# Kernel tuning notes

Measured on AMD Instinct MI355X. Metric: run time of the kernel, lower is better.

Reference implementation:

```python
import jax, jax.numpy as jnp
import numpy as np

D = 1024          # feature dim (x_dim)
C = 32            # n classes (way)
SHOTS = 32
N_SUP = C * SHOTS
Q = 1024
REG = 0.5         # reg_param


def setup_inputs() -> dict:
    key = jax.random.key(0)
    ks = jax.random.split(key, 5)
    support_x = jax.random.normal(ks[0], (N_SUP, D), dtype=jnp.float32)
    query_x = jax.random.normal(ks[1], (Q, D), dtype=jnp.float32)
    labels_idx = (jnp.arange(N_SUP, dtype=jnp.int32) % C)  # every class present, equal shots
    m = jax.random.normal(ks[2], (1, D), dtype=jnp.float32) * 0.01
    kappa = jnp.float32(0.1)
    nu = jnp.float32(D)
    triu_diag = jnp.ones((D,), dtype=jnp.float32)
    triu_lower = jnp.eye(D, dtype=jnp.float32) + 0.01 * jax.random.normal(ks[3], (D, D), dtype=jnp.float32)
    return {"support_x": support_x, "query_x": query_x, "labels_idx": labels_idx,
            "m": m, "kappa": kappa, "nu": nu,
            "triu_diag": triu_diag, "triu_lower": triu_lower}


def _metaqda_fb(support_x, query_x, labels_idx, m, kappa, nu, triu_diag, triu_lower):
    onehot = jax.nn.one_hot(labels_idx, C, dtype=support_x.dtype)      # [N, C]
    Nj = jnp.sum(onehot, axis=0)                                       # [C]
    kappa_ = jnp.abs(kappa) + 1e-6
    nu_ = jnp.maximum(nu, jnp.float32(D - 1 + 1e-6))

    # Cholesky-factor prior scatter matrix: L @ L^T
    lower_mask = jnp.tril(jnp.ones((D, D), dtype=support_x.dtype), k=-1)
    L = jnp.diag(jnp.abs(triu_diag)) + triu_lower * lower_mask
    prior_S = L @ L.T                                                  # [D, D]

    # per-class sums (replaces python loop of rank-1 outer products with GEMMs)
    sum_x = onehot.T @ support_x                                       # [C, D]
    mean_x = sum_x / Nj[:, None]
    # sum_n x x^T per class: contract through [N,C,D] intermediate
    SXX = jnp.einsum('nc,nd,ne->cde', onehot, support_x, support_x)    # [C, D, D]

    kN = kappa_ + Nj                                                   # [C]
    mu = (kappa_ / kN)[:, None] * m + (Nj / kN)[:, None] * mean_x      # [C, D]

    mm = m.T @ m                                                       # [D, D]  (self_outer of [1,D])
    mumu = jnp.einsum('cd,ce->cde', mu, mu)                            # [C, D, D]
    S = prior_S[None] + SXX + kappa_ * mm[None] - kN[:, None, None] * mumu

    scale = (kN + 1.0) / ((nu_ + Nj - D + 1.0) * kN)                   # [C]
    sigma = S * scale[:, None, None]                                   # [C, D, D]

    sigma_inv = (1.0 - REG) * jnp.linalg.inv(sigma) + REG * jnp.eye(D, dtype=sigma.dtype)

    common = nu_ + Nj + 1.0 - D                                        # [C]
    _, logdet = jnp.linalg.slogdet(sigma)
    bias = (jax.lax.lgamma(0.5 * (common + D)) - jax.lax.lgamma(0.5 * common)
            - 0.5 * D * jnp.log(common) - 0.5 * logdet)                # [C]

    diff = query_x[:, None, :] - mu[None, :, :]                        # [Q, C, D]
    dist = jnp.einsum('qcd,cde,qce->qc', diff, sigma_inv, diff)        # [Q, C]
    preds = bias[None, :] - 0.5 * (common + D)[None, :] * jnp.log1p(dist / common[None, :])
    return preds


def reference(support_x, query_x, labels_idx, m, kappa, nu, triu_diag, triu_lower):
    return _metaqda_fb(support_x, query_x, labels_idx, m, kappa, nu, triu_diag, triu_lower)
```

## Files before the change

### kernel.cpp

```cpp
#include <hip/hip_runtime.h>
#include <math.h>

#define Dk 1024
#define Ck 32
#define Nk 1024
#define Qk 1024
#define REGP 0.5f
#define NB 64
#define NROWSV (Qk + Nk + Ck + 1)

#define CO_KAPPA 0
#define CO_NU    1
#define CO_NJ    2
#define CO_KN    34
#define CO_SCALE 66
#define CO_COMMON 98
#define CO_COEF  130
#define CO_BIASA 162
#define CO_BIASF 200

#define O_P    0u
#define O_W    2162688u
#define O_T    3211264u
#define O_MU   3473408u
#define O_QM   3506176u
#define O_MB   3538944u
#define O_MI   3578112u
#define O_QNY  3617280u
#define O_QNO  3618304u
#define O_MUN  3619328u
#define O_GMM  3619360u
#define O_EX   3619392u
#define O_CONS 3619408u
#define O_CIDX 3619664u
#define O_YH   3652432u
#define O_YM   4733776u
#define O_YL   5815120u
#define O_WH   6896464u
#define O_WM   7420752u
#define O_WL   7945040u
#define O_OH   8469328u
#define O_OM   9550672u
#define O_OL   10632016u

#define WS_DECL \
    float* P     = Wbuf + O_P;    (void)P; \
    float* W     = Wbuf + O_W;    (void)W; \
    float* Tb    = Wbuf + O_T;    (void)Tb; \
    float* QM    = Wbuf + O_QM;   (void)QM; \
    float* Mbuf  = Wbuf + O_MB;   (void)Mbuf; \
    float* Minv  = Wbuf + O_MI;   (void)Minv; \
    float* qny   = Wbuf + O_QNY;  (void)qny; \
    float* qno   = Wbuf + O_QNO;  (void)qno; \
    float* mun2o = Wbuf + O_MUN;  (void)mun2o; \
    float* gmm   = Wbuf + O_GMM;  (void)gmm; \
    float* extraf= Wbuf + O_EX;   (void)extraf; \
    float* cons  = Wbuf + O_CONS; (void)cons; \
    int*   cidx  = (int*)(Wbuf + O_CIDX); (void)cidx; \
    ushort* sYh = (ushort*)(Wbuf + O_YH); (void)sYh; \
    ushort* sYm = (ushort*)(Wbuf + O_YM); (void)sYm; \
    ushort* sYl = (ushort*)(Wbuf + O_YL); (void)sYl; \
    ushort* sWh = (ushort*)(Wbuf + O_WH); (void)sWh; \
    ushort* sWm = (ushort*)(Wbuf + O_WM); (void)sWm; \
    ushort* sWl = (ushort*)(Wbuf + O_WL); (void)sWl; \
    ushort* sOh = (ushort*)(Wbuf + O_OH); (void)sOh; \
    ushort* sOm = (ushort*)(Wbuf + O_OM); (void)sOm; \
    ushort* sOl = (ushort*)(Wbuf + O_OL); (void)sOl;

typedef __attribute__((ext_vector_type(8))) __bf16 bf16x8;
typedef __attribute__((ext_vector_type(4))) float f32x4;

#define MFMA(a, b, c) __builtin_amdgcn_mfma_f32_16x16x32_bf16(a, b, c, 0, 0, 0)

__device__ __forceinline__ ushort f2bf(float x) {
    unsigned u = __float_as_uint(x);
    return (ushort)((u + 0x7FFFu + ((u >> 16) & 1u)) >> 16);
}
__device__ __forceinline__ float bf2f(ushort h) {
    return __uint_as_float(((unsigned)h) << 16);
}
__device__ __forceinline__ void split1(float x, ushort& h, ushort& m, ushort& l) {
    h = f2bf(x);
    float r1 = x - bf2f(h);
    m = f2bf(r1);
    l = f2bf(r1 - bf2f(m));
}
__device__ __forceinline__ void split_store4(ushort* ph, ushort* pm, ushort* pl,
                                             size_t o, float4 v) {
    float vv[4] = {v.x, v.y, v.z, v.w};
    ushort4 H, M, L;
    ushort* Hp = (ushort*)&H; ushort* Mp = (ushort*)&M; ushort* Lp = (ushort*)&L;
#pragma unroll
    for (int c = 0; c < 4; ++c) split1(vv[c], Hp[c], Mp[c], Lp[c]);
    *(ushort4*)(ph + o) = H;
    *(ushort4*)(pm + o) = M;
    *(ushort4*)(pl + o) = L;
}

__device__ __forceinline__ float wave_red(float s) {
#pragma unroll
    for (int o = 32; o > 0; o >>= 1) s += __shfl_down(s, o, 64);
    return s;
}

#define LDSB3(c, r, k8) ((c) * 5120 + (r) * 40 + (k8))
#define LDS_HW3 15360

__device__ __forceinline__ void b_fetch3(bf16x8* rb,
                                         const ushort* Bh, const ushort* Bm, const ushort* Bl,
                                         int bRow0, int kcol, int t) {
#pragma unroll
    for (int u = 0; u < 6; ++u) {
        int comp = u >> 1;
        int idx = ((u & 1) << 8) + t;
        int row = idx >> 2, kg = idx & 3;
        const ushort* Bs = (comp == 0) ? Bh : ((comp == 1) ? Bm : Bl);
        rb[u] = *(const bf16x8*)(Bs + (size_t)(bRow0 + row) * 1024 + kcol + kg * 8);
    }
}
__device__ __forceinline__ void b_store3(ushort* lds, const bf16x8* rb, int t) {
#pragma unroll
    for (int u = 0; u < 6; ++u) {
        int comp = u >> 1;
        int idx = ((u & 1) << 8) + t;
        int row = idx >> 2, kg = idx & 3;
        *(bf16x8*)(lds + LDSB3(comp, row, kg * 8)) = rb[u];
    }
}
__device__ __forceinline__ void a_fetch3(bf16x8 af[4][3],
                                         const ushort* Ah, const ushort* Am, const ushort* Al,
                                         int arowT, int aRowMax, int kcol, int lk) {
    bf16x8 z = {};
#pragma unroll
    for (int rf = 0; rf < 4; ++rf) {
        int gr = arowT + rf * 16;
        bool ok = gr < aRowMax;
#pragma unroll
        for (int c = 0; c < 3; ++c) {
            const ushort* As = (c == 0) ? Ah : ((c == 1) ? Am : Al);
            af[rf][c] = ok ? *(const bf16x8*)(As + (size_t)gr * 1024 + kcol + lk * 8) : z;
        }
    }
}

__device__ __forceinline__ void tile_compute3(const ushort* lds, f32x4 acc[4][4],
                                              bf16x8 af[4][3], int bcol0, int lr, int lk) {
#pragma unroll
    for (int cf = 0; cf < 4; ++cf) {
        int brow = bcol0 + cf * 16 + lr;
        bf16x8 bh = *(const bf16x8*)(lds + LDSB3(0, brow, lk * 8));
        bf16x8 bm = *(const bf16x8*)(lds + LDSB3(1, brow, lk * 8));
        bf16x8 bl = *(const bf16x8*)(lds + LDSB3(2, brow, lk * 8));
#pragma unroll
        for (int rf = 0; rf < 4; ++rf) {
            f32x4 a = acc[rf][cf];
            a = MFMA(af[rf][0], bh, a);
            a = MFMA(af[rf][0], bm, a);
            a = MFMA(af[rf][1], bh, a);
            a = MFMA(af[rf][0], bl, a);
            a = MFMA(af[rf][2], bh, a);
            a = MFMA(af[rf][1], bm, a);
            acc[rf][cf] = a;
        }
    }
}

__device__ __forceinline__ void tile_gemm3(
    ushort* lds, f32x4 acc[4][4],
    const ushort* Ah, const ushort* Am, const ushort* Al, int aRow0, int aRowMax,
    const ushort* Bh, const ushort* Bm, const ushort* Bl, int bRow0,
    int kbase, int ksteps, int t)
{
    const int w = t >> 6, lr = t & 15, lk = (t >> 4) & 3;
    const int arowT = aRow0 + (w >> 1) * 64 + lr;
    const int bcol0 = (w & 1) * 64;
    bf16x8 rb[6], afc[4][3], afn[4][3];
    b_fetch3(rb, Bh, Bm, Bl, bRow0, kbase * 32, t);
    a_fetch3(afc, Ah, Am, Al, arowT, aRowMax, kbase * 32, lk);
    b_store3(lds, rb, t);
    __syncthreads();
    for (int kt = 0; kt < ksteps; ++kt) {
        if (kt + 1 < ksteps) {
            b_fetch3(rb, Bh, Bm, Bl, bRow0, (kbase + kt + 1) * 32, t);
            a_fetch3(afn, Ah, Am, Al, arowT, aRowMax, (kbase + kt + 1) * 32, lk);
        }
        tile_compute3(lds, acc, afc, bcol0, lr, lk);
        __syncthreads();
        if (kt + 1 < ksteps) {
            b_store3(lds, rb, t);
#pragma unroll
            for (int rf = 0; rf < 4; ++rf)
#pragma unroll
                for (int c = 0; c < 3; ++c) afc[rf][c] = afn[rf][c];
        }
        __syncthreads();
    }
}

__device__ __forceinline__ void fetch4(float4* reg, const float* src, int ld,
                                       int rowbase, int rowmax, int colbase, int t) {
#pragma unroll
    for (int u = 0; u < 4; ++u) {
        int slot = t + u * 256;
        int r = slot >> 4, c4 = slot & 15;
        int gr = rowbase + r;
        reg[u] = (gr < rowmax) ? *(const float4*)(src + (size_t)gr * ld + colbase + c4 * 4)
                               : make_float4(0.f, 0.f, 0.f, 0.f);
    }
}
__device__ __forceinline__ void stT(float* dst, const float4* reg, int t) {
#pragma unroll
    for (int u = 0; u < 4; ++u) {
        int slot = t + u * 256;
        int r = slot >> 4, c4 = slot & 15;
        dst[(c4 * 4 + 0) * 68 + r] = reg[u].x;
        dst[(c4 * 4 + 1) * 68 + r] = reg[u].y;
        dst[(c4 * 4 + 2) * 68 + r] = reg[u].z;
        dst[(c4 * 4 + 3) * 68 + r] = reg[u].w;
    }
}
__device__ __forceinline__ void stN(float* dst, const float4* reg, int t) {
#pragma unroll
    for (int u = 0; u < 4; ++u) {
        int slot = t + u * 256;
        int r = slot >> 4, c4 = slot & 15;
        *(float4*)(dst + r * 68 + c4 * 4) = reg[u];
    }
}
__device__ __forceinline__ void gemm16(const float* At, const float* Bt,
                                       float acc[4][4], int tx, int ty) {
#pragma unroll 4
    for (int kk = 0; kk < NB; ++kk) {
        float4 a = *(const float4*)(At + kk * 68 + ty * 4);
        float4 b = *(const float4*)(Bt + kk * 68 + tx * 4);
        float av[4] = {a.x, a.y, a.z, a.w};
        float bv[4] = {b.x, b.y, b.z, b.w};
#pragma unroll
        for (int r = 0; r < 4; ++r)
#pragma unroll
            for (int s = 0; s < 4; ++s) acc[r][s] += av[r] * bv[s];
    }
}
__device__ __forceinline__ void mm_task(
    const float* aSrc, int aLd, int aRow, int aRowMax, int aCol, int aRowStep, int aColStep,
    const float* bSrc, int bLd, int bRow, int bRowMax, int bCol, int bRowStep, int bColStep,
    bool bTrans, int k0, int k1,
    float acc[4][4], float* smA, float* smB, int t, int tx, int ty)
{
    float4 ra[4], rb[4];
    fetch4(ra, aSrc, aLd, aRow + k0 * aRowStep, aRowMax, aCol + k0 * aColStep, t);
    fetch4(rb, bSrc, bLd, bRow + k0 * bRowStep, bRowMax, bCol + k0 * bColStep, t);
    stT(smA, ra, t);
    if (bTrans) stT(smB, rb, t); else stN(smB, rb, t);
    __syncthreads();
    for (int kt = k0; kt < k1; ++kt) {
        if (kt + 1 < k1) {
            fetch4(ra, aSrc, aLd, aRow + (kt + 1) * aRowStep, aRowMax, aCol + (kt + 1) * aColStep, t);
            fetch4(rb, bSrc, bLd, bRow + (kt + 1) * bRowStep, bRowMax, bCol + (kt + 1) * bColStep, t);
        }
        gemm16(smA, smB, acc, tx, ty);
        __syncthreads();
        if (kt + 1 < k1) {
            stT(smA, ra, t);
            if (bTrans) stT(smB, rb, t); else stN(smB, rb, t);
        }
        __syncthreads();
    }
}

__global__ __launch_bounds__(64) void k_tri0(const float* td, const float* tl, float* Wbuf) {
    __shared__ __align__(16) float smem[4416];
    WS_DECL
    const int t = threadIdx.x;
    int b0 = blockIdx.x * NB;
    float* LT   = smem;
    float* dinv = smem + 4352;
    for (int idx = t; idx < 64 * 64; idx += 64) {
        int m = idx >> 6, i = idx & 63;
        LT[i * 68 + m] = (m > i) ? tl[(size_t)(b0 + m) * Dk + b0 + i] : 0.f;
    }
    dinv[t] = 1.f / fabsf(td[b0 + t]);
    __syncthreads();
    const int j = t;
    float r[64];
#pragma unroll
    for (int m = 0; m < 64; ++m) r[m] = (m == j) ? 1.f : 0.f;
#pragma unroll
    for (int i = 0; i < 64; ++i) {
        float x = r[i] * dinv[i];
        r[i] = x;
#pragma unroll
        for (int g = (i >> 2); g < 16; ++g) {
            float4 lt = *(const float4*)&LT[i * 68 + g * 4];
            r[g * 4 + 0] -= lt.x * x;
            r[g * 4 + 1] -= lt.y * x;
            r[g * 4 + 2] -= lt.z * x;
            r[g * 4 + 3] -= lt.w * x;
        }
    }
#pragma unroll
    for (int i = 0; i < 64; ++i)
        W[(size_t)(b0 + i) * Dk + b0 + j] = r[i];
}

__global__ __launch_bounds__(256) void k_p0(const float* qx, const int* labels,
                                            const float* mvec, const float* kappa,
                                            const float* nu, const float* td,
                                            float* Wbuf) {
    __shared__ __align__(16) float sX[512];
    WS_DECL
    float* Yo32 = Wbuf;
    const int t = threadIdx.x;
    const int lane = t & 63, wv = t >> 6;
    const int tau = blockIdx.x;

    if (tau == 0) {
        int* scnt = (int*)sX;
        if (t < Ck) scnt[t] = 0;
        __syncthreads();
        for (int n = t; n < Nk; n += 256) {
            int l = labels[n];
            int pos = atomicAdd(&scnt[l], 1);
            cidx[l * Nk + pos] = n;
        }
        __syncthreads();
        if (t < Ck) {
            float kap = fabsf(kappa[0]) + 1e-6f;
            float nu_ = fmaxf(nu[0], (float)(Dk - 1) + 1e-6f);
            float Njf = (float)scnt[t];
            float kN = kap + Njf;
            if (t == 0) { cons[CO_KAPPA] = kap; cons[CO_NU] = nu_; }
            cons[CO_NJ + t] = Njf;
            cons[CO_KN + t] = kN;
            cons[CO_SCALE + t] = (kN + 1.0f) / ((nu_ + Njf - (float)Dk + 1.0f) * kN);
            float common = nu_ + Njf + 1.0f - (float)Dk;
            cons[CO_COMMON + t] = common;
            cons[CO_COEF + t] = 0.5f * (common + (float)Dk);
            cons[CO_BIASA + t] = lgammaf(0.5f * (common + (float)Dk)) - lgammaf(0.5f * common)
                                 - 0.5f * (float)Dk * logf(common);
        }
    } else if (tau == 1) {
        float s = 0.f;
        for (int i = t; i < Dk; i += 256) s += logf(fabsf(td[i]));
        s = wave_red(s);
        if (lane == 0) sX[wv] = s;
        __syncthreads();
        if (t == 0) extraf[0] = 2.f * (sX[0] + sX[1] + sX[2] + sX[3]);
    } else if (tau < 5) {
        int base = (tau - 2) * 13056;
        for (int i = t; i < 13056 && base + i < 39168; i += 256) Mbuf[base + i] = 0.f;
    } else if (tau == 5) {
        if (t < 32) { mun2o[t] = 0.f; gmm[t] = 0.f; }
        for (int i = t; i < 8192; i += 256)
            ((float4*)QM)[i] = make_float4(0, 0, 0, 0);
        if (t < 256) ((float4*)qny)[t] = make_float4(0, 0, 0, 0);
    } else if (tau < 70) {
        int rbase = (tau - 6) * 16;
        for (int j2 = wv; j2 < 16; j2 += 4) {
            const float* row = qx + (size_t)(rbase + j2) * Dk;
            float s = 0.f;
            for (int d = lane; d < Dk; d += 64) { float v = row[d]; s += v * v; }
            s = wave_red(s);
            if (lane == 0) qno[rbase + j2] = s;
        }
    } else if (tau < 134) {
        int rbase = (tau - 70) * 16;
        for (int j2 = 0; j2 < 16; ++j2) {
            int r = rbase + j2;
            float4 v = ((const float4*)(qx + (size_t)r * Dk))[t];
            split_store4(sYh, sYm, sYl, (size_t)r * 1024 + (size_t)t * 4, v);
        }
    } else if (tau == 134) {
        float4 v = ((const float4*)mvec)[t];
        split_store4(sYh, sYm, sYl, (size_t)2080 * 1024 + (size_t)t * 4, v);
    } else {
        int rbase = (tau - 135) * 16;
        for (int j2 = 0; j2 < 16; ++j2)
            ((float4*)(Yo32 + (size_t)(rbase + j2) * 1024))[t] = make_float4(0, 0, 0, 0);
    }
}

__global__ __launch_bounds__(256) void k_p1(const float* sx, const float* mvec,
                                            const float* tl, float* Wbuf) {
    __shared__ __align__(16) float smem[8704];
    WS_DECL
    const int t = threadIdx.x;
    const int lane = t & 63, wv = t >> 6;
    const int tau = blockIdx.x;
    if (tau < 128) {
        float* sX = smem;
        int c = tau >> 2;
        int d = ((tau & 3) << 8) + t;
        int Nj = (int)cons[CO_NJ + c];
        float kap = cons[CO_KAPPA], kN = cons[CO_KN + c];
        float acc = 0.f;
        for (int s = 0; s < Nj; ++s) acc += sx[(size_t)cidx[c * Nk + s] * Dk + d];
        float muv = (kap * mvec[d] + acc) / kN;
        size_t o = (size_t)(2048 + c) * 1024 + d;
        ushort h, m_, l_;
        split1(muv, h, m_, l_);
        sYh[o] = h; sYm[o] = m_; sYl[o] = l_;
        float s2 = wave_red(muv * muv);
        if (lane == 0) sX[wv] = s2;
        __syncthreads();
        if (t == 0) atomicAdd(&mun2o[c], sX[0] + sX[1] + sX[2] + sX[3]);
    } else if (tau < 192) {
        int rbase = (tau - 128) * 16;
        for (int j = 0; j < 16; ++j) {
            int n = rbase + j;
            int srcrow = cidx[(n >> 5) * Nk + (n & 31)];
            float4 v = ((const float4*)(sx + (size_t)srcrow * Dk))[t];
            split_store4(sYh, sYm, sYl, (size_t)(1024 + n) * 1024 + (size_t)t * 4, v);
        }
    } else {
        float* smA = smem;
        float* smB = smem + 4352;
        const int tx = t & 15, ty = t >> 4;
        const int BIG = 1 << 30;
        int pb = (tau - 192) * 128;
        float acc[4][4] = {};
        mm_task(tl, Dk, pb + 64, BIG, pb, 0, NB,
                W, Dk, pb, BIG, pb, NB, 0, false, 0, 1,
                acc, smA, smB, t, tx, ty);
        {
            float4 ra[4];
            fetch4(ra, W, Dk, pb + 64, BIG, pb + 64, t);
#pragma unroll
            for (int r = 0; r < 4; ++r)
#pragma unroll
                for (int s = 0; s < 4; ++s)
                    smB[(ty * 4 + r) * 68 + tx * 4 + s] = acc[r][s];
            stT(smA, ra, t);
        }
        __syncthreads();
        float acc2[4][4] = {};
        gemm16(smA, smB, acc2, tx, ty);
        __syncthreads();
#pragma unroll
        for (int r = 0; r < 4; ++r)
#pragma unroll
            for (int s = 0; s < 4; ++s)
                W[(size_t)(pb + 64 + ty * 4 + r) * Dk + pb + tx * 4 + s] = -acc2[r][s];
    }
}

__global__ __launch_bounds__(256) void k_tr_a(const float* tl, float* Wbuf, int h, int ht) {
    __shared__ __align__(16) float smem[8704];
    float* smA = smem;
    float* smB = smem + 4352;
    WS_DECL
    const int t = threadIdx.x;
    const int tx = t & 15, ty = t >> 4;
    const int BIG = 1 << 30;
    int tau = blockIdx.x;
    int p = tau / (ht * ht), rr = tau % (ht * ht);
    int i = rr / ht, j = rr % ht;
    int pb = p * 2 * h;
    float acc[4][4] = {};
    mm_task(tl, Dk, pb + h + i * NB, BIG, pb, 0, NB,
            W, Dk, pb, BIG, pb + j * NB, NB, 0, false, 0, ht,
            acc, smA, smB, t, tx, ty);
    float* Tp = Tb + (size_t)p * h * h;
#pragma unroll
    for (int r = 0; r < 4; ++r)
#pragma unroll
        for (int s = 0; s < 4; ++s)
            Tp[(size_t)(i * NB + ty * 4 + r) * h + j * NB + tx * 4 + s] = acc[r][s];
}

__global__ __launch_bounds__(256) void k_tr_b(float* Wbuf, int h, int ht) {
    __shared__ __align__(16) float smem[8704];
    float* smA = smem;
    float* smB = smem + 4352;
    WS_DECL
    const int t = threadIdx.x;
    const int tx = t & 15, ty = t >> 4;
    const int BIG = 1 << 30;
    int tau = blockIdx.x;
    int p = tau / (ht * ht), rr = tau % (ht * ht);
    int i = rr / ht, j = rr % ht;
    int pb = p * 2 * h;
    const float* Tp = Tb + (size_t)p * h * h;
    float acc[4][4] = {};
    mm_task(W, Dk, pb + h + i * NB, BIG, pb + h, 0, NB,
            Tp, h, 0, BIG, j * NB, NB, 0, false, 0, ht,
            acc, smA, smB, t, tx, ty);
#pragma unroll
    for (int r = 0; r < 4; ++r)
#pragma unroll
        for (int s = 0; s < 4; ++s)
            W[(size_t)(pb + h + i * NB + ty * 4 + r) * Dk + pb + j * NB + tx * 4 + s] = -acc[r][s];
}

__global__ __launch_bounds__(256) void k_cvtw(float* Wbuf) {
    WS_DECL
    const int t = threadIdx.x;
#pragma unroll
    for (int u = 0; u < 4; ++u) {
        unsigned g = blockIdx.x * 1024u + u * 256u + t;
        int row = g >> 8, col4 = (g & 255) * 4;
        float4 v = ((const float4*)W)[g];
        if (col4 + 0 > row) v.x = 0.f;
        if (col4 + 1 > row) v.y = 0.f;
        if (col4 + 2 > row) v.z = 0.f;
        if (col4 + 3 > row) v.w = 0.f;
        split_store4(sWh, sWm, sWl, (size_t)g * 4, v);
    }
}

__global__ __launch_bounds__(256) void k_yg(float* Wbuf) {
    __shared__ __align__(16) ushort lds[LDS_HW3];
    WS_DECL
    float* Yo32 = Wbuf;
    const int t = threadIdx.x;
    int b = blockIdx.x;
    int xcd = b & 7, pos = b >> 3;
    int e = (xcd < 4) ? xcd * 43 + pos : 172 + (xcd - 4) * 42 + pos;
    int q = e / 17, rt = e % 17;
    int jt2, kc;
    if (q < 4)       { jt2 = 7; kc = q; }
    else if (q < 8)  { jt2 = 6; kc = q - 4; }
    else if (q < 11) { jt2 = 5; kc = q - 8; }
    else if (q < 14) { jt2 = 4; kc = q - 11; }
    else if (q < 16) { jt2 = 3; kc = q - 14; }
    else if (q < 18) { jt2 = 2; kc = q - 16; }
    else if (q == 18){ jt2 = 1; kc = 0; }
    else             { jt2 = 0; kc = 0; }
    int ksteps = min(8, 4 * (jt2 + 1) - kc * 8);
    f32x4 acc[4][4] = {};
    tile_gemm3(lds, acc, sYh, sYm, sYl, rt * 128, 2081,
               sWh, sWm, sWl, jt2 * 128, kc * 8, ksteps, t);
    const int w = t >> 6, lr = t & 15, lk = (t >> 4) & 3;
#pragma unroll
    for (int rf = 0; rf < 4; ++rf)
#pragma unroll
        for (int cf = 0; cf < 4; ++cf)
#pragma unroll
            for (int r = 0; r < 4; ++r) {
                int grow = rt * 128 + (w >> 1) * 64 + rf * 16 + lk * 4 + r;
                if (grow < NROWSV)
                    atomicAdd(&Yo32[(size_t)grow * 1024 + jt2 * 128 + (w & 1) * 64 + cf * 16 + lr],
                              acc[rf][cf][r]);
            }
}

__global__ __launch_bounds__(256) void k_cvto(float* Wbuf) {
    __shared__ float sred[16];
    WS_DECL
    float* Yo32 = Wbuf;
    const int t = threadIdx.x;
    const int lane = t & 63, wv = t >> 6;
    int rbase = blockIdx.x * 4;
    float4 vv[4];
#pragma unroll
    for (int j = 0; j < 4; ++j) {
        int r = rbase + j;
        float4 v = ((const float4*)(Yo32 + (size_t)r * 1024))[t];
        vv[j] = v;
        split_store4(sOh, sOm, sOl, (size_t)r * 1024 + (size_t)t * 4, v);
    }
    if (rbase < 1024) {
#pragma unroll
        for (int j = 0; j < 4; ++j) {
            float4 v = vv[j];
            float s = v.x * v.x + v.y * v.y + v.z * v.z + v.w * v.w;
            s = wave_red(s);
            if (lane == 0) sred[wv * 4 + j] = s;
        }
        __syncthreads();
        if (t < 4)
            qny[rbase + t] = sred[t] + sred[4 + t] + sred[8 + t] + sred[12 + t];
    }
    if (rbase < 1088) {
#pragma unroll
        for (int j = 0; j < 4; ++j)
            ((float4*)(Yo32 + (size_t)(rbase + j) * 1024))[t] = make_float4(0, 0, 0, 0);
    }
}

__global__ __launch_bounds__(256) void k_p4m(float* Wbuf) {
    __shared__ __align__(16) ushort lds[LDS_HW3];
    WS_DECL
    const int t = threadIdx.x;
    int b = blockIdx.x;
    int e = (b & 7) * 40 + (b >> 3);
    const int w = t >> 6, lr = t & 15, lk = (t >> 4) & 3;
    f32x4 acc[4][4] = {};
    if (e < 288) {
        int qt2 = e / 36, rem = e % 36;
        int mt = rem >> 2, kc = rem & 3;
        tile_gemm3(lds, acc, sOh, sOm, sOl, 1024 + mt * 128, 2081,
                   sOh, sOm, sOl, qt2 * 128, kc * 8, 8, t);
#pragma unroll
        for (int rf = 0; rf < 4; ++rf)
#pragma unroll
            for (int cf = 0; cf < 4; ++cf)
#pragma unroll
                for (int r = 0; r < 4; ++r) {
                    int n = mt * 128 + (w >> 1) * 64 + rf * 16 + lk * 4 + r;
                    if (n < Nk + Ck + 1)
                        atomicAdd(&P[(size_t)n * 1024 + qt2 * 128 + (w & 1) * 64 + cf * 16 + lr],
                                  acc[rf][cf][r]);
                }
    } else {
        int f = e - 288;
        int qt2 = f >> 2, kc = f & 3;
        tile_gemm3(lds, acc, sYh, sYm, sYl, 2048, 2080,
                   sYh, sYm, sYl, qt2 * 128, kc * 8, 8, t);
#pragma unroll
        for (int rf = 0; rf < 4; ++rf)
#pragma unroll
            for (int cf = 0; cf < 4; ++cf)
#pragma unroll
                for (int r = 0; r < 4; ++r) {
                    int rq = (w >> 1) * 64 + rf * 16 + lk * 4 + r;
                    if (rq < 32)
                        atomicAdd(&QM[(size_t)rq * 1024 + qt2 * 128 + (w & 1) * 64 + cf * 16 + lr],
                                  acc[rf][cf][r]);
                }
    }
}

__global__ __launch_bounds__(256) void k_gram(float* Wbuf) {
    __shared__ __align__(16) float smA[34 * 68];
    WS_DECL
    const int t = threadIdx.x;
    const int tau = blockIdx.x;
    int c = tau >> 2, kc = tau & 3;
    float accg[5];
    int iu[5], ju[5];
#pragma unroll
    for (int u = 0; u < 5; ++u) {
        int e = t + u * 256;
        iu[u] = e / 34; ju[u] = e - iu[u] * 34;
        accg[u] = 0.f;
    }
    for (int kt = kc * 4; kt < kc * 4 + 4; ++kt) {
        for (int e2 = t; e2 < 34 * NB; e2 += 256) {
            int i = e2 >> 6, k = e2 & 63;
            int yr = (i < 32) ? (Qk + c * 32 + i) : ((i == 32) ? (Qk + Nk + c) : (Qk + Nk + Ck));
            size_t o = (size_t)yr * 1024 + kt * NB + k;
            smA[i * 68 + k] = bf2f(sOh[o]) + bf2f(sOm[o]) + bf2f(sOl[o]);
        }
        __syncthreads();
#pragma unroll
        for (int u = 0; u < 5; ++u) {
            int e = t + u * 256;
            if (e < 1156) {
                float s = 0.f;
                for (int k = 0; k < NB; ++k) s += smA[iu[u] * 68 + k] * smA[ju[u] * 68 + k];
                accg[u] += s;
            }
        }
        __syncthreads();
    }
#pragma unroll
    for (int u = 0; u < 5; ++u) {
        int e = t + u * 256;
        if (e < 1156)
            atomicAdd(&Mbuf[c * 1224 + iu[u] * 36 + ju[u]], accg[u]);
    }
}

__global__ __launch_bounds__(64) void k_p5(float* Wbuf) {
    __shared__ __align__(16) float A[34 * 36];
    WS_DECL
    const int t = threadIdx.x;
    const int c = blockIdx.x;
    float kN = cons[CO_KN + c], kap = cons[CO_KAPPA];
    for (int e = t; e < 34 * 34; e += 64) {
        int i = e / 34, j = e - i * 34;
        A[i * 36 + j] = Mbuf[c * 1224 + i * 36 + j];
    }
    __syncthreads();
    if (t == 0) {
        gmm[c] = A[32 * 36 + 32];
        A[32 * 36 + 32] += -1.f / kN;
        A[33 * 36 + 33] += 1.f / kap;
    }
    if (t < 32) A[t * 36 + t] += 1.f;
    __syncthreads();
    float ldacc = 0.f;
    for (int j = 0; j < 34; ++j) {
        float piv = A[j * 36 + j];
        float pinv = 1.f / piv;
        if (t == 0) ldacc += logf(fabsf(piv));
        if (t < 34 && t != j) A[j * 36 + t] *= pinv;
        __syncthreads();
        if (t < 34) {
            if (t != j) {
                float f = A[t * 36 + j];
                float4* rowT = (float4*)(A + t * 36);
                const float4* rowJ = (const float4*)(A + j * 36);
#pragma unroll
                for (int k4 = 0; k4 < 8; ++k4) {
                    float4 rv = rowT[k4], pv = rowJ[k4];
                    rv.x -= f * pv.x; rv.y -= f * pv.y;
                    rv.z -= f * pv.z; rv.w -= f * pv.w;
                    rowT[k4] = rv;
                }
                A[t * 36 + 32] -= f * A[j * 36 + 32];
                A[t * 36 + 33] -= f * A[j * 36 + 33];
                A[t * 36 + j] = -f * pinv;
            } else {
                A[j * 36 + j] = pinv;
            }
        }
        __syncthreads();
    }
    for (int e = t; e < 34 * 34; e += 64) {
        int i = e / 34, j = e - i * 34;
        Minv[c * 1224 + i * 36 + j] = A[i * 36 + j];
    }
    if (t == 0) {
        float scale = cons[CO_SCALE + c];
        float logdet = (float)Dk * logf(scale) + extraf[0] + logf(kN) + logf(kap) + ldacc;
        cons[CO_BIASF + c] = cons[CO_BIASA + c] - 0.5f * logdet;
    }
}

__global__ __launch_bounds__(256) void k_p6(float* Wbuf, float* out) {
    __shared__ __align__(16) float smem[3904];
    float* Mi  = smem;
    float* wL  = smem + 1200;
    float* gsm = smem + 3520;
    float* red = smem + 3520 + 128;
    WS_DECL
    const int t = threadIdx.x;
    const int tau = blockIdx.x;
    int qt = tau >> 5, c = tau & 31;
    for (int e = t; e < 34 * 34; e += 256) {
        int i = e / 34, j = e - i * 34;
        Mi[i * 35 + j] = Minv[c * 1224 + i * 36 + j];
    }
    if (t < 34)
        gsm[t] = (t < 32) ? Mbuf[c * 1224 + t * 36 + 32]
                          : ((t == 32) ? gmm[c] : Mbuf[c * 1224 + 33 * 36 + 32]);
    __syncthreads();
    for (int e = t; e < 34 * NB; e += 256) {
        int i = e >> 6, qq = e & 63;
        int prow = (i < 32) ? (c * 32 + i) : ((i == 32) ? (Nk + c) : (Nk + Ck));
        wL[i * 68 + qq] = P[(size_t)prow * Qk + qt * NB + qq] - gsm[i];
    }
    __syncthreads();
    {
        int q = t & 63, part = t >> 6;
        int start = (part < 2) ? part * 9 : 18 + (part - 2) * 8;
        int cnt = (part < 2) ? 9 : 8;
        float partial = 0.f;
        for (int i = start; i < start + cnt; ++i) {
            float v = 0.f;
            for (int j = 0; j < 34; ++j) v += Mi[i * 35 + j] * wL[j * 68 + q];
            partial += v * wL[i * 68 + q];
        }
        red[part * 64 + q] = partial;
    }
    __syncthreads();
    if (t < 64) {
        int q = t;
        float quad = red[q] + red[64 + q] + red[128 + q] + red[192 + q];
        int qg = qt * NB + q;
        float w32 = wL[32 * 68 + q];
        float ydist2 = qny[qg] - 2.f * w32 - gmm[c];
        float dd = qno[qg] + mun2o[c] - 2.f * QM[(size_t)c * Qk + qg];
        float scale = cons[CO_SCALE + c], common = cons[CO_COMMON + c];
        float dist = (1.f - REGP) / scale * (ydist2 - quad) + REGP * dd;
        out[(size_t)qg * Ck + c] = cons[CO_BIASF + c] - cons[CO_COEF + c] * log1pf(dist / common);
    }
}

extern "C" void kernel_launch(void* const* d_in, const int* in_sizes, int n_in,
                              void* d_out, int out_size, void* d_ws, size_t ws_size,
                              hipStream_t stream) {
    const float* sx = (const float*)d_in[0];
    const float* qx = (const float*)d_in[1];
    const int* labels = (const int*)d_in[2];
    const float* mvec = (const float*)d_in[3];
    const float* kappa = (const float*)d_in[4];
    const float* nu = (const float*)d_in[5];
    const float* td = (const float*)d_in[6];
    const float* tl = (const float*)d_in[7];
    float* W = (float*)d_ws;
    float* out = (float*)d_out;

    hipLaunchKernelGGL(k_p0, dim3(267), dim3(256), 0, stream,
                       qx, labels, mvec, kappa, nu, td, W);
    hipLaunchKernelGGL(k_tri0, dim3(16), dim3(64), 0, stream, td, tl, W);
    hipLaunchKernelGGL(k_p1, dim3(200), dim3(256), 0, stream, sx, mvec, tl, W);
    for (int l = 2; l <= 4; ++l) {
        int h = 32 << l, ht = h >> 6, pairs = 16 >> l;
        int nt = pairs * ht * ht;
        hipLaunchKernelGGL(k_tr_a, dim3(nt), dim3(256), 0, stream, tl, W, h, ht);
        hipLaunchKernelGGL(k_tr_b, dim3(nt), dim3(256), 0, stream, W, h, ht);
    }
    hipLaunchKernelGGL(k_cvtw, dim3(256), dim3(256), 0, stream, W);
    hipLaunchKernelGGL(k_yg, dim3(340), dim3(256), 0, stream, W);
    hipLaunchKernelGGL(k_cvto, dim3(528), dim3(256), 0, stream, W);
    hipLaunchKernelGGL(k_p4m, dim3(320), dim3(256), 0, stream, W);
    hipLaunchKernelGGL(k_gram, dim3(128), dim3(256), 0, stream, W);
    hipLaunchKernelGGL(k_p5, dim3(32), dim3(64), 0, stream, W);
    hipLaunchKernelGGL(k_p6, dim3(512), dim3(256), 0, stream, W, out);
}
```

Measured before the change: 373.7 us.

## Move query-row norm reduction into gram kernel and drop XCD block remapping

```diff
diff --git a/kernel.cpp b/kernel.cpp
--- a/kernel.cpp
+++ b/kernel.cpp
@@ -353,7 +353,6 @@
         if (t < 32) { mun2o[t] = 0.f; gmm[t] = 0.f; }
         for (int i = t; i < 8192; i += 256)
             ((float4*)QM)[i] = make_float4(0, 0, 0, 0);
-        if (t < 256) ((float4*)qny)[t] = make_float4(0, 0, 0, 0);
     } else if (tau < 70) {
         int rbase = (tau - 6) * 16;
         for (int j2 = wv; j2 < 16; j2 += 4) {
@@ -513,9 +512,7 @@
     WS_DECL
     float* Yo32 = Wbuf;
     const int t = threadIdx.x;
-    int b = blockIdx.x;
-    int xcd = b & 7, pos = b >> 3;
-    int e = (xcd < 4) ? xcd * 43 + pos : 172 + (xcd - 4) * 42 + pos;
+    int e = blockIdx.x;
     int q = e / 17, rt = e % 17;
     int jt2, kc;
     if (q < 4)       { jt2 = 7; kc = q; }
@@ -545,31 +542,15 @@
 }
 
 __global__ __launch_bounds__(256) void k_cvto(float* Wbuf) {
-    __shared__ float sred[16];
     WS_DECL
     float* Yo32 = Wbuf;
     const int t = threadIdx.x;
-    const int lane = t & 63, wv = t >> 6;
     int rbase = blockIdx.x * 4;
-    float4 vv[4];
 #pragma unroll
     for (int j = 0; j < 4; ++j) {
         int r = rbase + j;
         float4 v = ((const float4*)(Yo32 + (size_t)r * 1024))[t];
-        vv[j] = v;
         split_store4(sOh, sOm, sOl, (size_t)r * 1024 + (size_t)t * 4, v);
-    }
-    if (rbase < 1024) {
-#pragma unroll
-        for (int j = 0; j < 4; ++j) {
-            float4 v = vv[j];
-            float s = v.x * v.x + v.y * v.y + v.z * v.z + v.w * v.w;
-            s = wave_red(s);
-            if (lane == 0) sred[wv * 4 + j] = s;
-        }
-        __syncthreads();
-        if (t < 4)
-            qny[rbase + t] = sred[t] + sred[4 + t] + sred[8 + t] + sred[12 + t];
     }
     if (rbase < 1088) {
 #pragma unroll
@@ -582,13 +563,12 @@
     __shared__ __align__(16) ushort lds[LDS_HW3];
     WS_DECL
     const int t = threadIdx.x;
-    int b = blockIdx.x;
-    int e = (b & 7) * 40 + (b >> 3);
+    int e = blockIdx.x;
     const int w = t >> 6, lr = t & 15, lk = (t >> 4) & 3;
     f32x4 acc[4][4] = {};
     if (e < 288) {
-        int qt2 = e / 36, rem = e % 36;
-        int mt = rem >> 2, kc = rem & 3;
+        int tile = e >> 2, kc = e & 3;
+        int mt = tile >> 3, qt2 = tile & 7;
         tile_gemm3(lds, acc, sOh, sOm, sOl, 1024 + mt * 128, 2081,
                    sOh, sOm, sOl, qt2 * 128, kc * 8, 8, t);
 #pragma unroll
@@ -625,40 +605,56 @@
     __shared__ __align__(16) float smA[34 * 68];
     WS_DECL
     const int t = threadIdx.x;
+    const int lane = t & 63, wv = t >> 6;
     const int tau = blockIdx.x;
-    int c = tau >> 2, kc = tau & 3;
-    float accg[5];
-    int iu[5], ju[5];
-#pragma unroll
-    for (int u = 0; u < 5; ++u) {
-        int e = t + u * 256;
-        iu[u] = e / 34; ju[u] = e - iu[u] * 34;
-        accg[u] = 0.f;
-    }
-    for (int kt = kc * 4; kt < kc * 4 + 4; ++kt) {
-        for (int e2 = t; e2 < 34 * NB; e2 += 256) {
-            int i = e2 >> 6, k = e2 & 63;
-            int yr = (i < 32) ? (Qk + c * 32 + i) : ((i == 32) ? (Qk + Nk + c) : (Qk + Nk + Ck));
-            size_t o = (size_t)yr * 1024 + kt * NB + k;
-            smA[i * 68 + k] = bf2f(sOh[o]) + bf2f(sOm[o]) + bf2f(sOl[o]);
-        }
-        __syncthreads();
+    if (tau < 128) {
+        int c = tau >> 2, kc = tau & 3;
+        float accg[5];
+        int iu[5], ju[5];
 #pragma unroll
         for (int u = 0; u < 5; ++u) {
             int e = t + u * 256;
-            if (e < 1156) {
-                float s = 0.f;
-                for (int k = 0; k < NB; ++k) s += smA[iu[u] * 68 + k] * smA[ju[u] * 68 + k];
-                accg[u] += s;
+            iu[u] = e / 34; ju[u] = e - iu[u] * 34;
+            accg[u] = 0.f;
+        }
+        for (int kt = kc * 4; kt < kc * 4 + 4; ++kt) {
+            for (int e2 = t; e2 < 34 * NB; e2 += 256) {
+                int i = e2 >> 6, k = e2 & 63;
+                int yr = (i < 32) ? (Qk + c * 32 + i) : ((i == 32) ? (Qk + Nk + c) : (Qk + Nk + Ck));
+                size_t o = (size_t)yr * 1024 + kt * NB + k;
+                smA[i * 68 + k] = bf2f(sOh[o]) + bf2f(sOm[o]) + bf2f(sOl[o]);
             }
-        }
-        __syncthreads();
-    }
-#pragma unroll
-    for (int u = 0; u < 5; ++u) {
-        int e = t + u * 256;
-        if (e < 1156)
-            atomicAdd(&Mbuf[c * 1224 + iu[u] * 36 + ju[u]], accg[u]);
+            __syncthreads();
+#pragma unroll
+            for (int u = 0; u < 5; ++u) {
+                int e = t + u * 256;
+                if (e < 1156) {
+                    float s = 0.f;
+                    for (int k = 0; k < NB; ++k) s += smA[iu[u] * 68 + k] * smA[ju[u] * 68 + k];
+                    accg[u] += s;
+                }
+            }
+            __syncthreads();
+        }
+#pragma unroll
+        for (int u = 0; u < 5; ++u) {
+            int e = t + u * 256;
+            if (e < 1156)
+                atomicAdd(&Mbuf[c * 1224 + iu[u] * 36 + ju[u]], accg[u]);
+        }
+    } else {
+        int rbase = (tau - 128) * 16;
+        for (int j = wv; j < 16; j += 4) {
+            size_t ro = (size_t)(rbase + j) * 1024;
+            float s = 0.f;
+            for (int d = lane; d < Dk; d += 64) {
+                size_t o = ro + d;
+                float v = bf2f(sOh[o]) + bf2f(sOm[o]) + bf2f(sOl[o]);
+                s += v * v;
+            }
+            s = wave_red(s);
+            if (lane == 0) qny[rbase + j] = s;
+        }
     }
 }
 
@@ -783,9 +779,9 @@
     float* W = (float*)d_ws;
     float* out = (float*)d_out;
 
+    hipLaunchKernelGGL(k_tri0, dim3(16), dim3(64), 0, stream, td, tl, W);
     hipLaunchKernelGGL(k_p0, dim3(267), dim3(256), 0, stream,
                        qx, labels, mvec, kappa, nu, td, W);
-    hipLaunchKernelGGL(k_tri0, dim3(16), dim3(64), 0, stream, td, tl, W);
     hipLaunchKernelGGL(k_p1, dim3(200), dim3(256), 0, stream, sx, mvec, tl, W);
     for (int l = 2; l <= 4; ++l) {
         int h = 32 << l, ht = h >> 6, pairs = 16 >> l;
@@ -797,7 +793,7 @@
     hipLaunchKernelGGL(k_yg, dim3(340), dim3(256), 0, stream, W);
     hipLaunchKernelGGL(k_cvto, dim3(528), dim3(256), 0, stream, W);
     hipLaunchKernelGGL(k_p4m, dim3(320), dim3(256), 0, stream, W);
-    hipLaunchKernelGGL(k_gram, dim3(128), dim3(256), 0, stream, W);
+    hipLaunchKernelGGL(k_gram, dim3(192), dim3(256), 0, stream, W);
     hipLaunchKernelGGL(k_p5, dim3(32), dim3(64), 0, stream, W);
     hipLaunchKernelGGL(k_p6, dim3(512), dim3(256), 0, stream, W, out);
 }
```

New measurement: 371.8 us. No clear change (-0.5%).
